# Kernel tuning notes

Measured on AMD Instinct MI355X. Metric: run time of the kernel, lower is better.

The kernel has to match this reference:

```python
import jax, jax.numpy as jnp
import numpy as np

BS, H, S, DK = 4, 16, 1024, 64  # bs, n_heads, seq_len(=q_len), head_dim


def setup_inputs() -> dict:
    key = jax.random.key(0)
    k1, k2, k3, k4 = jax.random.split(key, 4)
    return {
        "q": jax.random.normal(k1, (BS, H, S, DK), dtype=jnp.float32),
        "k": jax.random.normal(k2, (BS, H, DK, S), dtype=jnp.float32),
        "v": jax.random.normal(k3, (BS, H, S, DK), dtype=jnp.float32),
        "prev": jax.random.normal(k4, (BS, H, S, S), dtype=jnp.float32),
        "attn_mask": jnp.zeros((1, S, S), dtype=jnp.float32),  # additive float mask
        "key_padding_mask": jnp.zeros((BS, S), dtype=bool),     # True = masked key
        "scale": jnp.asarray(DK ** -0.5, dtype=jnp.float32),    # learnable (lsa=True)
    }


def reference(q, k, v, prev, attn_mask, key_padding_mask, scale):
    # attn_scores = q @ k * scale + prev + attn_mask (float branch)
    scores = jnp.einsum("bhqd,bhdk->bhqk", q, k) * scale
    scores = scores + prev + attn_mask[:, None, :, :]  # [1,S,S] -> broadcast over b,h
    # key_padding_mask: [bs, seq_len] -> masked_fill(-inf)
    scores = jnp.where(key_padding_mask[:, None, None, :], -jnp.inf, scores)
    attn = jax.nn.softmax(scores, axis=-1)  # dropout p=0.0 -> identity
    out = jnp.einsum("bhqk,bhkd->bhqd", attn, v)
    # res_attention=True -> (output, attn_weights, attn_scores)
    return out, attn, scores
```

## Files before the change

kernel.cpp:

```cpp
#include <hip/hip_runtime.h>
#include <math.h>

#define SEQ 1024
#define DKH 64
#define QBLK 64
#define NTILE 16
#define KSTR 68
#define ESTR 1032

typedef short s8v __attribute__((ext_vector_type(8)));
typedef short s4v __attribute__((ext_vector_type(4)));
typedef float f4v __attribute__((ext_vector_type(4)));

__device__ __forceinline__ short f2bf(float f) {
    unsigned u = __builtin_bit_cast(unsigned, f);
    return (short)((u + 0x8000u) >> 16);
}
__device__ __forceinline__ float bf2f(unsigned short h) {
    unsigned u = ((unsigned)h) << 16;
    return __builtin_bit_cast(float, u);
}
__device__ __forceinline__ s8v ld_frag(const unsigned short* p) {
    s4v a = *(const s4v*)(p);
    s4v b = *(const s4v*)(p + 4);
    s8v r;
    r[0]=a[0]; r[1]=a[1]; r[2]=a[2]; r[3]=a[3];
    r[4]=b[0]; r[5]=b[1]; r[6]=b[2]; r[7]=b[3];
    return r;
}

__global__ __launch_bounds__(256, 1)
void attn_fused(const float* __restrict__ q, const float* __restrict__ k,
                const float* __restrict__ v, const float* __restrict__ prev,
                const float* __restrict__ mask, const unsigned char* __restrict__ kpm,
                const float* __restrict__ scale_p,
                float* __restrict__ out, float* __restrict__ attn,
                float* __restrict__ scores)
{
    __shared__ unsigned short e_s[QBLK * ESTR];
    __shared__ unsigned short k_s[64 * KSTR];
    __shared__ unsigned short v_s[64 * KSTR];
    __shared__ float inv_s[QBLK];

    const int t   = threadIdx.x;
    const int w   = t >> 6;
    const int l   = t & 63;
    const int g   = l >> 4;
    const int c16 = l & 15;
    const int sa  = t & 15, sg = t >> 4;

    const int wg  = blockIdx.x;
    const int swz = (wg & 7) * 128 + (wg >> 3);
    const int bh  = swz >> 4;
    const int rt  = swz & 15;
    const int b   = bh >> 4;

    const float scale = *scale_p;

    const float* qb = q    + ((size_t)bh * SEQ + rt * QBLK) * DKH;
    const float* kb = k    + (size_t)bh * DKH * SEQ;
    const float* vb = v    + (size_t)bh * SEQ * DKH;
    const float* pb = prev + ((size_t)bh * SEQ + rt * QBLK) * SEQ;
    const float* mb = mask + (size_t)(rt * QBLK) * SEQ;
    const unsigned char* kp = kpm + (size_t)b * SEQ;
    float* sb = scores + ((size_t)bh * SEQ + rt * QBLK) * SEQ;
    float* ab = attn   + ((size_t)bh * SEQ + rt * QBLK) * SEQ;
    float* ob = out    + ((size_t)bh * SEQ + rt * QBLK) * DKH;

    {
        const int row = t >> 2, c0 = (t & 3) * 16;
        const float* src = qb + row * DKH + c0;
        #pragma unroll
        for (int j = 0; j < 4; ++j) {
            f4v f = *(const f4v*)(src + 4 * j);
            s4v h; h[0]=f2bf(f[0]); h[1]=f2bf(f[1]); h[2]=f2bf(f[2]); h[3]=f2bf(f[3]);
            *(s4v*)&e_s[row * ESTR + c0 + 4 * j] = h;
        }
    }
    __syncthreads();

    s8v aq[2];
    aq[0] = ld_frag(&e_s[(w * 16 + c16) * ESTR + g * 8]);
    aq[1] = ld_frag(&e_s[(w * 16 + c16) * ESTR + 32 + g * 8]);

    f4v kreg[4], vreg[4];
    auto load_k = [&](int ct) {
        const float* src = kb + (size_t)(4 * sg) * SEQ + ct * 64 + 4 * sa;
        kreg[0] = *(const f4v*)(src);
        kreg[1] = *(const f4v*)(src + SEQ);
        kreg[2] = *(const f4v*)(src + 2 * SEQ);
        kreg[3] = *(const f4v*)(src + 3 * SEQ);
    };
    auto load_v = [&](int ct) {
        const float* src = vb + (size_t)(ct * 64 + 4 * sg) * DKH + 4 * sa;
        vreg[0] = *(const f4v*)(src);
        vreg[1] = *(const f4v*)(src + DKH);
        vreg[2] = *(const f4v*)(src + 2 * DKH);
        vreg[3] = *(const f4v*)(src + 3 * DKH);
    };
    auto load_pm = [&](int ct, float (&pr)[16], float (&mr)[16]) {
        #pragma unroll
        for (int r = 0; r < 4; ++r) {
            const float* prow = pb + (size_t)(w * 16 + 4 * g + r) * SEQ + ct * 64 + c16;
            const float* mrow = mb + (size_t)(w * 16 + 4 * g + r) * SEQ + ct * 64 + c16;
            #pragma unroll
            for (int s = 0; s < 4; ++s) {
                pr[r * 4 + s] = __builtin_nontemporal_load(prow + s * 16);
                mr[r * 4 + s] = mrow[s * 16];
            }
        }
    };

    float l_r[4] = {0.f, 0.f, 0.f, 0.f};
    f4v oacc[4];
    #pragma unroll
    for (int d = 0; d < 4; ++d) oacc[d] = 0;

    float prA[16], mrA[16], prB[16], mrB[16];
    load_k(0); load_v(0);
    load_pm(0, prA, mrA);

    auto tile_body = [&](int ct, float (&prc)[16], float (&mrc)[16],
                         float (&prn)[16], float (&mrn)[16]) {
        __syncthreads();
        #pragma unroll
        for (int j = 0; j < 4; ++j) {
            s4v hk; hk[0]=f2bf(kreg[0][j]); hk[1]=f2bf(kreg[1][j]); hk[2]=f2bf(kreg[2][j]); hk[3]=f2bf(kreg[3][j]);
            *(s4v*)&k_s[(4 * sa + j) * KSTR + 4 * sg] = hk;
            s4v hv; hv[0]=f2bf(vreg[0][j]); hv[1]=f2bf(vreg[1][j]); hv[2]=f2bf(vreg[2][j]); hv[3]=f2bf(vreg[3][j]);
            *(s4v*)&v_s[(4 * sa + j) * KSTR + 4 * sg] = hv;
        }
        __syncthreads();

        if (ct + 1 < NTILE) {
            load_k(ct + 1); load_v(ct + 1);
            load_pm(ct + 1, prn, mrn);
        }

        f4v acc[4];
        #pragma unroll
        for (int s = 0; s < 4; ++s) acc[s] = 0;
        #pragma unroll
        for (int ks = 0; ks < 2; ++ks) {
            #pragma unroll
            for (int s = 0; s < 4; ++s) {
                s8v bk = ld_frag(&k_s[(s * 16 + c16) * KSTR + ks * 32 + g * 8]);
                acc[s] = __builtin_amdgcn_mfma_f32_16x16x32_bf16(aq[ks], bk, acc[s], 0, 0, 0);
            }
        }

        const int colb = ct * 64;
        int kf[4];
        #pragma unroll
        for (int s = 0; s < 4; ++s) kf[s] = kp[colb + s * 16 + c16];

        float ev[16];
        #pragma unroll
        for (int r = 0; r < 4; ++r) {
            float* srow = sb + (size_t)(w * 16 + 4 * g + r) * SEQ + colb + c16;
            #pragma unroll
            for (int s = 0; s < 4; ++s) {
                float x = fmaf(acc[s][r], scale, prc[r * 4 + s] + mrc[r * 4 + s]);
                x = kf[s] ? -INFINITY : x;
                __builtin_nontemporal_store(x, srow + s * 16);
                const float e = __expf(x);
                ev[r * 4 + s] = e;
                l_r[r] += e;
            }
        }
        #pragma unroll
        for (int r = 0; r < 4; ++r) {
            #pragma unroll
            for (int s = 0; s < 4; ++s)
                e_s[(w * 16 + 4 * g + r) * ESTR + colb + s * 16 + c16] =
                    (unsigned short)f2bf(ev[r * 4 + s]);
        }
        #pragma unroll
        for (int cs = 0; cs < 2; ++cs) {
            s8v ae = ld_frag(&e_s[(w * 16 + c16) * ESTR + colb + cs * 32 + g * 8]);
            #pragma unroll
            for (int d = 0; d < 4; ++d) {
                s8v bv = ld_frag(&v_s[(d * 16 + c16) * KSTR + cs * 32 + g * 8]);
                oacc[d] = __builtin_amdgcn_mfma_f32_16x16x32_bf16(ae, bv, oacc[d], 0, 0, 0);
            }
        }
    };

    for (int ct2 = 0; ct2 < NTILE; ct2 += 2) {
        tile_body(ct2,     prA, mrA, prB, mrB);
        tile_body(ct2 + 1, prB, mrB, prA, mrA);
    }

    #pragma unroll
    for (int off = 1; off <= 8; off <<= 1) {
        #pragma unroll
        for (int r = 0; r < 4; ++r) l_r[r] += __shfl_xor(l_r[r], off, 64);
    }
    float inv_r[4];
    #pragma unroll
    for (int r = 0; r < 4; ++r) inv_r[r] = 1.0f / l_r[r];
    if (c16 == 0) {
        #pragma unroll
        for (int r = 0; r < 4; ++r) inv_s[w * 16 + 4 * g + r] = inv_r[r];
    }

    const int rsub = l >> 4;
    #pragma unroll
    for (int rr = 0; rr < 4; ++rr) {
        const int row = w * 16 + rr * 4 + rsub;
        const float inv = inv_s[row];
        float* arow = ab + (size_t)row * SEQ;
        const unsigned short* erow = &e_s[row * ESTR];
        #pragma unroll
        for (int j = 0; j < 8; ++j) {
            const int c0 = j * 128 + c16 * 8;
            s8v h = ld_frag(erow + c0);
            f4v a0, a1;
            #pragma unroll
            for (int u = 0; u < 4; ++u) {
                a0[u] = bf2f((unsigned short)h[u]) * inv;
                a1[u] = bf2f((unsigned short)h[4 + u]) * inv;
            }
            __builtin_nontemporal_store(a0, (f4v*)(arow + c0));
            __builtin_nontemporal_store(a1, (f4v*)(arow + c0 + 4));
        }
    }

    #pragma unroll
    for (int d = 0; d < 4; ++d) {
        #pragma unroll
        for (int r = 0; r < 4; ++r)
            __builtin_nontemporal_store(oacc[d][r] * inv_r[r],
                ob + (size_t)(w * 16 + 4 * g + r) * DKH + d * 16 + c16);
    }
}

extern "C" void kernel_launch(void* const* d_in, const int* in_sizes, int n_in,
                              void* d_out, int out_size, void* d_ws, size_t ws_size,
                              hipStream_t stream) {
    const float* q    = (const float*)d_in[0];
    const float* k    = (const float*)d_in[1];
    const float* v    = (const float*)d_in[2];
    const float* prev = (const float*)d_in[3];
    const float* mask = (const float*)d_in[4];
    const unsigned char* kpm = (const unsigned char*)d_in[5];
    const float* scale = (const float*)d_in[6];

    float* out    = (float*)d_out;
    float* attn   = out  + (size_t)4 * 16 * SEQ * DKH;
    float* scores = attn + (size_t)4 * 16 * SEQ * SEQ;

    attn_fused<<<dim3(1024), dim3(256), 0, stream>>>(q, k, v, prev, mask, kpm, scale,
                                                     out, attn, scores);
}
```

Before: 294.5 us.

## Halve query block, use 8 waves splitting columns, load K/V fragments directly

```diff
diff --git a/kernel.cpp b/kernel.cpp
--- a/kernel.cpp
+++ b/kernel.cpp
@@ -3,10 +3,9 @@
 
 #define SEQ 1024
 #define DKH 64
-#define QBLK 64
+#define QBLK 32
 #define NTILE 16
-#define KSTR 68
-#define ESTR 1032
+#define ESTR 1028
 
 typedef short s8v __attribute__((ext_vector_type(8)));
 typedef short s4v __attribute__((ext_vector_type(4)));
@@ -29,7 +28,7 @@
     return r;
 }
 
-__global__ __launch_bounds__(256, 1)
+__global__ __launch_bounds__(512, 4)
 void attn_fused(const float* __restrict__ q, const float* __restrict__ k,
                 const float* __restrict__ v, const float* __restrict__ prev,
                 const float* __restrict__ mask, const unsigned char* __restrict__ kpm,
@@ -38,21 +37,21 @@
                 float* __restrict__ scores)
 {
     __shared__ unsigned short e_s[QBLK * ESTR];
-    __shared__ unsigned short k_s[64 * KSTR];
-    __shared__ unsigned short v_s[64 * KSTR];
+    __shared__ float l_part[QBLK][4];
     __shared__ float inv_s[QBLK];
 
     const int t   = threadIdx.x;
     const int w   = t >> 6;
+    const int rg  = w >> 2;
+    const int cq  = w & 3;
     const int l   = t & 63;
     const int g   = l >> 4;
     const int c16 = l & 15;
-    const int sa  = t & 15, sg = t >> 4;
 
     const int wg  = blockIdx.x;
-    const int swz = (wg & 7) * 128 + (wg >> 3);
-    const int bh  = swz >> 4;
-    const int rt  = swz & 15;
+    const int swz = (wg & 7) * 256 + (wg >> 3);
+    const int bh  = swz >> 5;
+    const int rt  = swz & 31;
     const int b   = bh >> 4;
 
     const float scale = *scale_p;
@@ -68,127 +67,92 @@
     float* ob = out    + ((size_t)bh * SEQ + rt * QBLK) * DKH;
 
     {
-        const int row = t >> 2, c0 = (t & 3) * 16;
-        const float* src = qb + row * DKH + c0;
-        #pragma unroll
-        for (int j = 0; j < 4; ++j) {
-            f4v f = *(const f4v*)(src + 4 * j);
-            s4v h; h[0]=f2bf(f[0]); h[1]=f2bf(f[1]); h[2]=f2bf(f[2]); h[3]=f2bf(f[3]);
-            *(s4v*)&e_s[row * ESTR + c0 + 4 * j] = h;
+        const int row = t >> 4, c0 = (t & 15) * 4;
+        f4v f = *(const f4v*)(qb + row * DKH + c0);
+        s4v h; h[0]=f2bf(f[0]); h[1]=f2bf(f[1]); h[2]=f2bf(f[2]); h[3]=f2bf(f[3]);
+        *(s4v*)&e_s[row * ESTR + c0] = h;
+    }
+    __syncthreads();
+
+    const s8v aq0 = ld_frag(&e_s[(rg * 16 + c16) * ESTR + g * 8]);
+    const s8v aq1 = ld_frag(&e_s[(rg * 16 + c16) * ESTR + 32 + g * 8]);
+    __syncthreads();
+
+    const float* kcol = kb + (size_t)(g * 8) * SEQ + cq * 16 + c16;
+    const float* vcol = vb + (size_t)(g * 8) * DKH + cq * 16 + c16;
+    const float* prow0 = pb + (size_t)(rg * 16 + g * 4) * SEQ + cq * 16 + c16;
+    const float* mrow0 = mb + (size_t)(rg * 16 + g * 4) * SEQ + cq * 16 + c16;
+
+    float kraw[16], vraw[16];
+    auto load_K = [&](int ct) {
+        const float* p0 = kcol + ct * 64;
+        #pragma unroll
+        for (int ks = 0; ks < 2; ++ks)
+            #pragma unroll
+            for (int e = 0; e < 8; ++e)
+                kraw[ks * 8 + e] = p0[(size_t)(ks * 32 + e) * SEQ];
+    };
+    auto load_V = [&](int ct) {
+        const float* p0 = vcol + (size_t)(ct * 64) * DKH;
+        #pragma unroll
+        for (int cs = 0; cs < 2; ++cs)
+            #pragma unroll
+            for (int e = 0; e < 8; ++e)
+                vraw[cs * 8 + e] = p0[(size_t)(cs * 32 + e) * DKH];
+    };
+    auto load_PM = [&](int ct, float (&pr)[4], float (&mr)[4], int& kf) {
+        #pragma unroll
+        for (int r = 0; r < 4; ++r) {
+            pr[r] = __builtin_nontemporal_load(prow0 + (size_t)r * SEQ + ct * 64);
+            mr[r] = mrow0[(size_t)r * SEQ + ct * 64];
         }
-    }
-    __syncthreads();
-
-    s8v aq[2];
-    aq[0] = ld_frag(&e_s[(w * 16 + c16) * ESTR + g * 8]);
-    aq[1] = ld_frag(&e_s[(w * 16 + c16) * ESTR + 32 + g * 8]);
-
-    f4v kreg[4], vreg[4];
-    auto load_k = [&](int ct) {
-        const float* src = kb + (size_t)(4 * sg) * SEQ + ct * 64 + 4 * sa;
-        kreg[0] = *(const f4v*)(src);
-        kreg[1] = *(const f4v*)(src + SEQ);
-        kreg[2] = *(const f4v*)(src + 2 * SEQ);
-        kreg[3] = *(const f4v*)(src + 3 * SEQ);
-    };
-    auto load_v = [&](int ct) {
-        const float* src = vb + (size_t)(ct * 64 + 4 * sg) * DKH + 4 * sa;
-        vreg[0] = *(const f4v*)(src);
-        vreg[1] = *(const f4v*)(src + DKH);
-        vreg[2] = *(const f4v*)(src + 2 * DKH);
-        vreg[3] = *(const f4v*)(src + 3 * DKH);
-    };
-    auto load_pm = [&](int ct, float (&pr)[16], float (&mr)[16]) {
+        kf = kp[ct * 64 + cq * 16 + c16];
+    };
+
+    float l_r[4] = {0.f, 0.f, 0.f, 0.f};
+    f4v oacc = 0;
+
+    float prA[4], mrA[4], prB[4], mrB[4];
+    int kfA = 0, kfB = 0;
+    load_K(0); load_V(0); load_PM(0, prA, mrA, kfA);
+
+    auto tile = [&](int ct, float (&prc)[4], float (&mrc)[4], int kfc,
+                    float (&prn)[4], float (&mrn)[4], int& kfn) {
+        s8v ka, kb2;
+        #pragma unroll
+        for (int e = 0; e < 8; ++e) { ka[e] = f2bf(kraw[e]); kb2[e] = f2bf(kraw[8 + e]); }
+        f4v acc = 0;
+        acc = __builtin_amdgcn_mfma_f32_16x16x32_bf16(aq0, ka,  acc, 0, 0, 0);
+        acc = __builtin_amdgcn_mfma_f32_16x16x32_bf16(aq1, kb2, acc, 0, 0, 0);
+        if (ct + 1 < NTILE) load_K(ct + 1);
+
+        const int colb = ct * 64 + cq * 16 + c16;
         #pragma unroll
         for (int r = 0; r < 4; ++r) {
-            const float* prow = pb + (size_t)(w * 16 + 4 * g + r) * SEQ + ct * 64 + c16;
-            const float* mrow = mb + (size_t)(w * 16 + 4 * g + r) * SEQ + ct * 64 + c16;
-            #pragma unroll
-            for (int s = 0; s < 4; ++s) {
-                pr[r * 4 + s] = __builtin_nontemporal_load(prow + s * 16);
-                mr[r * 4 + s] = mrow[s * 16];
-            }
+            const int row = rg * 16 + g * 4 + r;
+            float x = fmaf(acc[r], scale, prc[r] + mrc[r]);
+            x = kfc ? -INFINITY : x;
+            __builtin_nontemporal_store(x, sb + (size_t)row * SEQ + colb);
+            const float e = __expf(x);
+            l_r[r] += e;
+            e_s[row * ESTR + colb] = (unsigned short)f2bf(e);
         }
-    };
-
-    float l_r[4] = {0.f, 0.f, 0.f, 0.f};
-    f4v oacc[4];
-    #pragma unroll
-    for (int d = 0; d < 4; ++d) oacc[d] = 0;
-
-    float prA[16], mrA[16], prB[16], mrB[16];
-    load_k(0); load_v(0);
-    load_pm(0, prA, mrA);
-
-    auto tile_body = [&](int ct, float (&prc)[16], float (&mrc)[16],
-                         float (&prn)[16], float (&mrn)[16]) {
+        if (ct + 1 < NTILE) load_PM(ct + 1, prn, mrn, kfn);
         __syncthreads();
-        #pragma unroll
-        for (int j = 0; j < 4; ++j) {
-            s4v hk; hk[0]=f2bf(kreg[0][j]); hk[1]=f2bf(kreg[1][j]); hk[2]=f2bf(kreg[2][j]); hk[3]=f2bf(kreg[3][j]);
-            *(s4v*)&k_s[(4 * sa + j) * KSTR + 4 * sg] = hk;
-            s4v hv; hv[0]=f2bf(vreg[0][j]); hv[1]=f2bf(vreg[1][j]); hv[2]=f2bf(vreg[2][j]); hv[3]=f2bf(vreg[3][j]);
-            *(s4v*)&v_s[(4 * sa + j) * KSTR + 4 * sg] = hv;
-        }
-        __syncthreads();
-
-        if (ct + 1 < NTILE) {
-            load_k(ct + 1); load_v(ct + 1);
-            load_pm(ct + 1, prn, mrn);
-        }
-
-        f4v acc[4];
-        #pragma unroll
-        for (int s = 0; s < 4; ++s) acc[s] = 0;
-        #pragma unroll
-        for (int ks = 0; ks < 2; ++ks) {
-            #pragma unroll
-            for (int s = 0; s < 4; ++s) {
-                s8v bk = ld_frag(&k_s[(s * 16 + c16) * KSTR + ks * 32 + g * 8]);
-                acc[s] = __builtin_amdgcn_mfma_f32_16x16x32_bf16(aq[ks], bk, acc[s], 0, 0, 0);
-            }
-        }
-
-        const int colb = ct * 64;
-        int kf[4];
-        #pragma unroll
-        for (int s = 0; s < 4; ++s) kf[s] = kp[colb + s * 16 + c16];
-
-        float ev[16];
-        #pragma unroll
-        for (int r = 0; r < 4; ++r) {
-            float* srow = sb + (size_t)(w * 16 + 4 * g + r) * SEQ + colb + c16;
-            #pragma unroll
-            for (int s = 0; s < 4; ++s) {
-                float x = fmaf(acc[s][r], scale, prc[r * 4 + s] + mrc[r * 4 + s]);
-                x = kf[s] ? -INFINITY : x;
-                __builtin_nontemporal_store(x, srow + s * 16);
-                const float e = __expf(x);
-                ev[r * 4 + s] = e;
-                l_r[r] += e;
-            }
-        }
-        #pragma unroll
-        for (int r = 0; r < 4; ++r) {
-            #pragma unroll
-            for (int s = 0; s < 4; ++s)
-                e_s[(w * 16 + 4 * g + r) * ESTR + colb + s * 16 + c16] =
-                    (unsigned short)f2bf(ev[r * 4 + s]);
-        }
-        #pragma unroll
-        for (int cs = 0; cs < 2; ++cs) {
-            s8v ae = ld_frag(&e_s[(w * 16 + c16) * ESTR + colb + cs * 32 + g * 8]);
-            #pragma unroll
-            for (int d = 0; d < 4; ++d) {
-                s8v bv = ld_frag(&v_s[(d * 16 + c16) * KSTR + cs * 32 + g * 8]);
-                oacc[d] = __builtin_amdgcn_mfma_f32_16x16x32_bf16(ae, bv, oacc[d], 0, 0, 0);
-            }
-        }
-    };
-
-    for (int ct2 = 0; ct2 < NTILE; ct2 += 2) {
-        tile_body(ct2,     prA, mrA, prB, mrB);
-        tile_body(ct2 + 1, prB, mrB, prA, mrA);
+
+        const s8v ae0 = ld_frag(&e_s[(rg * 16 + c16) * ESTR + ct * 64 + g * 8]);
+        const s8v ae1 = ld_frag(&e_s[(rg * 16 + c16) * ESTR + ct * 64 + 32 + g * 8]);
+        s8v va, vb2;
+        #pragma unroll
+        for (int e = 0; e < 8; ++e) { va[e] = f2bf(vraw[e]); vb2[e] = f2bf(vraw[8 + e]); }
+        oacc = __builtin_amdgcn_mfma_f32_16x16x32_bf16(ae0, va,  oacc, 0, 0, 0);
+        oacc = __builtin_amdgcn_mfma_f32_16x16x32_bf16(ae1, vb2, oacc, 0, 0, 0);
+        if (ct + 1 < NTILE) load_V(ct + 1);
+    };
+
+    for (int c2 = 0; c2 < NTILE; c2 += 2) {
+        tile(c2,     prA, mrA, kfA, prB, mrB, kfB);
+        tile(c2 + 1, prB, mrB, kfB, prA, mrA, kfA);
     }
 
     #pragma unroll
@@ -196,24 +160,30 @@
         #pragma unroll
         for (int r = 0; r < 4; ++r) l_r[r] += __shfl_xor(l_r[r], off, 64);
     }
-    float inv_r[4];
+    if (c16 == 0) {
+        #pragma unroll
+        for (int r = 0; r < 4; ++r) l_part[rg * 16 + g * 4 + r][cq] = l_r[r];
+    }
+    __syncthreads();
+    if (t < QBLK)
+        inv_s[t] = 1.0f / (l_part[t][0] + l_part[t][1] + l_part[t][2] + l_part[t][3]);
+    __syncthreads();
+
     #pragma unroll
-    for (int r = 0; r < 4; ++r) inv_r[r] = 1.0f / l_r[r];
-    if (c16 == 0) {
-        #pragma unroll
-        for (int r = 0; r < 4; ++r) inv_s[w * 16 + 4 * g + r] = inv_r[r];
-    }
-
-    const int rsub = l >> 4;
-    #pragma unroll
-    for (int rr = 0; rr < 4; ++rr) {
-        const int row = w * 16 + rr * 4 + rsub;
+    for (int r = 0; r < 4; ++r) {
+        const int row = rg * 16 + g * 4 + r;
+        __builtin_nontemporal_store(oacc[r] * inv_s[row],
+            ob + (size_t)row * DKH + cq * 16 + c16);
+    }
+
+    {
+        const int row = t >> 4, i = t & 15;
         const float inv = inv_s[row];
+        const unsigned short* erow = &e_s[row * ESTR];
         float* arow = ab + (size_t)row * SEQ;
-        const unsigned short* erow = &e_s[row * ESTR];
         #pragma unroll
         for (int j = 0; j < 8; ++j) {
-            const int c0 = j * 128 + c16 * 8;
+            const int c0 = (j * 16 + i) * 8;
             s8v h = ld_frag(erow + c0);
             f4v a0, a1;
             #pragma unroll
@@ -225,14 +195,6 @@
             __builtin_nontemporal_store(a1, (f4v*)(arow + c0 + 4));
         }
     }
-
-    #pragma unroll
-    for (int d = 0; d < 4; ++d) {
-        #pragma unroll
-        for (int r = 0; r < 4; ++r)
-            __builtin_nontemporal_store(oacc[d][r] * inv_r[r],
-                ob + (size_t)(w * 16 + 4 * g + r) * DKH + d * 16 + c16);
-    }
 }
 
 extern "C" void kernel_launch(void* const* d_in, const int* in_sizes, int n_in,
@@ -250,6 +212,6 @@
     float* attn   = out  + (size_t)4 * 16 * SEQ * DKH;
     float* scores = attn + (size_t)4 * 16 * SEQ * SEQ;
 
-    attn_fused<<<dim3(1024), dim3(256), 0, stream>>>(q, k, v, prev, mask, kpm, scale,
+    attn_fused<<<dim3(2048), dim3(512), 0, stream>>>(q, k, v, prev, mask, kpm, scale,
                                                      out, attn, scores);
 }
```

New measurement: 326.5 us. 1.11x slower.

## Split fused attention into QK-scores kernel and PV/attn kernel for occupancy

Applied to the files above, without the earlier changes.

```diff
diff --git a/kernel.cpp b/kernel.cpp
--- a/kernel.cpp
+++ b/kernel.cpp
@@ -6,7 +6,6 @@
 #define QBLK 64
 #define NTILE 16
 #define KSTR 68
-#define ESTR 1032
 
 typedef short s8v __attribute__((ext_vector_type(8)));
 typedef short s4v __attribute__((ext_vector_type(4)));
@@ -15,10 +14,6 @@
 __device__ __forceinline__ short f2bf(float f) {
     unsigned u = __builtin_bit_cast(unsigned, f);
     return (short)((u + 0x8000u) >> 16);
-}
-__device__ __forceinline__ float bf2f(unsigned short h) {
-    unsigned u = ((unsigned)h) << 16;
-    return __builtin_bit_cast(float, u);
 }
 __device__ __forceinline__ s8v ld_frag(const unsigned short* p) {
     s4v a = *(const s4v*)(p);
@@ -29,18 +24,14 @@
     return r;
 }
 
-__global__ __launch_bounds__(256, 1)
-void attn_fused(const float* __restrict__ q, const float* __restrict__ k,
-                const float* __restrict__ v, const float* __restrict__ prev,
-                const float* __restrict__ mask, const unsigned char* __restrict__ kpm,
-                const float* __restrict__ scale_p,
-                float* __restrict__ out, float* __restrict__ attn,
-                float* __restrict__ scores)
+__global__ __launch_bounds__(256, 3)
+void qk_scores(const float* __restrict__ q, const float* __restrict__ k,
+               const float* __restrict__ prev, const float* __restrict__ mask,
+               const unsigned char* __restrict__ kpm, const float* __restrict__ scale_p,
+               float* __restrict__ scores, float* __restrict__ inv_ws)
 {
-    __shared__ unsigned short e_s[QBLK * ESTR];
+    __shared__ unsigned short q_s[QBLK * KSTR];
     __shared__ unsigned short k_s[64 * KSTR];
-    __shared__ unsigned short v_s[64 * KSTR];
-    __shared__ float inv_s[QBLK];
 
     const int t   = threadIdx.x;
     const int w   = t >> 6;
@@ -59,13 +50,10 @@
 
     const float* qb = q    + ((size_t)bh * SEQ + rt * QBLK) * DKH;
     const float* kb = k    + (size_t)bh * DKH * SEQ;
-    const float* vb = v    + (size_t)bh * SEQ * DKH;
     const float* pb = prev + ((size_t)bh * SEQ + rt * QBLK) * SEQ;
     const float* mb = mask + (size_t)(rt * QBLK) * SEQ;
     const unsigned char* kp = kpm + (size_t)b * SEQ;
     float* sb = scores + ((size_t)bh * SEQ + rt * QBLK) * SEQ;
-    float* ab = attn   + ((size_t)bh * SEQ + rt * QBLK) * SEQ;
-    float* ob = out    + ((size_t)bh * SEQ + rt * QBLK) * DKH;
 
     {
         const int row = t >> 2, c0 = (t & 3) * 16;
@@ -74,31 +62,22 @@
         for (int j = 0; j < 4; ++j) {
             f4v f = *(const f4v*)(src + 4 * j);
             s4v h; h[0]=f2bf(f[0]); h[1]=f2bf(f[1]); h[2]=f2bf(f[2]); h[3]=f2bf(f[3]);
-            *(s4v*)&e_s[row * ESTR + c0 + 4 * j] = h;
+            *(s4v*)&q_s[row * KSTR + c0 + 4 * j] = h;
         }
     }
     __syncthreads();
-
-    s8v aq[2];
-    aq[0] = ld_frag(&e_s[(w * 16 + c16) * ESTR + g * 8]);
-    aq[1] = ld_frag(&e_s[(w * 16 + c16) * ESTR + 32 + g * 8]);
-
-    f4v kreg[4], vreg[4];
-    auto load_k = [&](int ct) {
+    const s8v aq0 = ld_frag(&q_s[(w * 16 + c16) * KSTR + g * 8]);
+    const s8v aq1 = ld_frag(&q_s[(w * 16 + c16) * KSTR + 32 + g * 8]);
+
+    f4v kreg[4];
+    auto load_K = [&](int ct) {
         const float* src = kb + (size_t)(4 * sg) * SEQ + ct * 64 + 4 * sa;
         kreg[0] = *(const f4v*)(src);
         kreg[1] = *(const f4v*)(src + SEQ);
         kreg[2] = *(const f4v*)(src + 2 * SEQ);
         kreg[3] = *(const f4v*)(src + 3 * SEQ);
     };
-    auto load_v = [&](int ct) {
-        const float* src = vb + (size_t)(ct * 64 + 4 * sg) * DKH + 4 * sa;
-        vreg[0] = *(const f4v*)(src);
-        vreg[1] = *(const f4v*)(src + DKH);
-        vreg[2] = *(const f4v*)(src + 2 * DKH);
-        vreg[3] = *(const f4v*)(src + 3 * DKH);
-    };
-    auto load_pm = [&](int ct, float (&pr)[16], float (&mr)[16]) {
+    auto load_PM = [&](int ct, float (&pr)[16], float (&mr)[16], int (&kf)[4]) {
         #pragma unroll
         for (int r = 0; r < 4; ++r) {
             const float* prow = pb + (size_t)(w * 16 + 4 * g + r) * SEQ + ct * 64 + c16;
@@ -109,121 +88,163 @@
                 mr[r * 4 + s] = mrow[s * 16];
             }
         }
+        #pragma unroll
+        for (int s = 0; s < 4; ++s) kf[s] = kp[ct * 64 + s * 16 + c16];
     };
 
     float l_r[4] = {0.f, 0.f, 0.f, 0.f};
-    f4v oacc[4];
-    #pragma unroll
-    for (int d = 0; d < 4; ++d) oacc[d] = 0;
-
     float prA[16], mrA[16], prB[16], mrB[16];
-    load_k(0); load_v(0);
-    load_pm(0, prA, mrA);
-
-    auto tile_body = [&](int ct, float (&prc)[16], float (&mrc)[16],
-                         float (&prn)[16], float (&mrn)[16]) {
+    int kfA[4], kfB[4];
+    load_K(0);
+    load_PM(0, prA, mrA, kfA);
+
+    auto tile = [&](int ct, float (&prc)[16], float (&mrc)[16], int (&kfc)[4],
+                    float (&prn)[16], float (&mrn)[16], int (&kfn)[4]) {
         __syncthreads();
         #pragma unroll
         for (int j = 0; j < 4; ++j) {
             s4v hk; hk[0]=f2bf(kreg[0][j]); hk[1]=f2bf(kreg[1][j]); hk[2]=f2bf(kreg[2][j]); hk[3]=f2bf(kreg[3][j]);
             *(s4v*)&k_s[(4 * sa + j) * KSTR + 4 * sg] = hk;
-            s4v hv; hv[0]=f2bf(vreg[0][j]); hv[1]=f2bf(vreg[1][j]); hv[2]=f2bf(vreg[2][j]); hv[3]=f2bf(vreg[3][j]);
-            *(s4v*)&v_s[(4 * sa + j) * KSTR + 4 * sg] = hv;
-        }
-        __syncthreads();
-
-        if (ct + 1 < NTILE) {
-            load_k(ct + 1); load_v(ct + 1);
-            load_pm(ct + 1, prn, mrn);
-        }
+        }
+        __syncthreads();
+
+        if (ct + 1 < NTILE) load_K(ct + 1);
 
         f4v acc[4];
         #pragma unroll
         for (int s = 0; s < 4; ++s) acc[s] = 0;
         #pragma unroll
-        for (int ks = 0; ks < 2; ++ks) {
-            #pragma unroll
-            for (int s = 0; s < 4; ++s) {
-                s8v bk = ld_frag(&k_s[(s * 16 + c16) * KSTR + ks * 32 + g * 8]);
-                acc[s] = __builtin_amdgcn_mfma_f32_16x16x32_bf16(aq[ks], bk, acc[s], 0, 0, 0);
-            }
-        }
+        for (int s = 0; s < 4; ++s) {
+            const s8v bk0 = ld_frag(&k_s[(s * 16 + c16) * KSTR + g * 8]);
+            acc[s] = __builtin_amdgcn_mfma_f32_16x16x32_bf16(aq0, bk0, acc[s], 0, 0, 0);
+            const s8v bk1 = ld_frag(&k_s[(s * 16 + c16) * KSTR + 32 + g * 8]);
+            acc[s] = __builtin_amdgcn_mfma_f32_16x16x32_bf16(aq1, bk1, acc[s], 0, 0, 0);
+        }
+
+        if (ct + 1 < NTILE) load_PM(ct + 1, prn, mrn, kfn);
 
         const int colb = ct * 64;
-        int kf[4];
-        #pragma unroll
-        for (int s = 0; s < 4; ++s) kf[s] = kp[colb + s * 16 + c16];
-
-        float ev[16];
         #pragma unroll
         for (int r = 0; r < 4; ++r) {
             float* srow = sb + (size_t)(w * 16 + 4 * g + r) * SEQ + colb + c16;
             #pragma unroll
             for (int s = 0; s < 4; ++s) {
                 float x = fmaf(acc[s][r], scale, prc[r * 4 + s] + mrc[r * 4 + s]);
-                x = kf[s] ? -INFINITY : x;
-                __builtin_nontemporal_store(x, srow + s * 16);
-                const float e = __expf(x);
-                ev[r * 4 + s] = e;
-                l_r[r] += e;
+                x = kfc[s] ? -INFINITY : x;
+                srow[s * 16] = x;
+                l_r[r] += __expf(x);
             }
         }
+    };
+
+    for (int c2 = 0; c2 < NTILE; c2 += 2) {
+        tile(c2,     prA, mrA, kfA, prB, mrB, kfB);
+        tile(c2 + 1, prB, mrB, kfB, prA, mrA, kfA);
+    }
+
+    #pragma unroll
+    for (int off = 1; off <= 8; off <<= 1) {
+        #pragma unroll
+        for (int r = 0; r < 4; ++r) l_r[r] += __shfl_xor(l_r[r], off, 64);
+    }
+    if (c16 == 0) {
+        #pragma unroll
+        for (int r = 0; r < 4; ++r)
+            inv_ws[(size_t)bh * SEQ + rt * QBLK + w * 16 + 4 * g + r] = 1.0f / l_r[r];
+    }
+}
+
+__global__ __launch_bounds__(256, 3)
+void pv_attn(const float* __restrict__ v, const float* __restrict__ scores,
+             const float* __restrict__ inv_ws,
+             float* __restrict__ attn, float* __restrict__ out)
+{
+    __shared__ unsigned short v_s[64 * KSTR];
+    __shared__ unsigned short e_s[4][16 * KSTR];
+
+    const int t   = threadIdx.x;
+    const int w   = t >> 6;
+    const int l   = t & 63;
+    const int g   = l >> 4;
+    const int c16 = l & 15;
+    const int sa  = t & 15, sg = t >> 4;
+
+    const int wg  = blockIdx.x;
+    const int swz = (wg & 7) * 128 + (wg >> 3);
+    const int bh  = swz >> 4;
+    const int rt  = swz & 15;
+
+    const float* vb  = v      + (size_t)bh * SEQ * DKH;
+    const float* sbr = scores + ((size_t)bh * SEQ + rt * QBLK) * SEQ;
+    float* ab = attn + ((size_t)bh * SEQ + rt * QBLK) * SEQ;
+    float* ob = out  + ((size_t)bh * SEQ + rt * QBLK) * DKH;
+
+    float inv_r[4];
+    #pragma unroll
+    for (int r = 0; r < 4; ++r)
+        inv_r[r] = inv_ws[(size_t)bh * SEQ + rt * QBLK + w * 16 + g * 4 + r];
+
+    f4v vreg[4];
+    auto load_V = [&](int ct) {
+        const float* src = vb + (size_t)(ct * 64 + 4 * sg) * DKH + 4 * sa;
+        vreg[0] = *(const f4v*)(src);
+        vreg[1] = *(const f4v*)(src + DKH);
+        vreg[2] = *(const f4v*)(src + 2 * DKH);
+        vreg[3] = *(const f4v*)(src + 3 * DKH);
+    };
+    auto load_S = [&](int ct, f4v (&sr)[4]) {
+        #pragma unroll
+        for (int r = 0; r < 4; ++r)
+            sr[r] = *(const f4v*)(sbr + (size_t)(w * 16 + g * 4 + r) * SEQ + ct * 64 + c16 * 4);
+    };
+
+    f4v oacc[4];
+    #pragma unroll
+    for (int d = 0; d < 4; ++d) oacc[d] = 0;
+
+    f4v sregA[4], sregB[4];
+    load_V(0);
+    load_S(0, sregA);
+
+    auto tile = [&](int ct, f4v (&sc)[4], f4v (&sn)[4]) {
+        __syncthreads();
+        #pragma unroll
+        for (int j = 0; j < 4; ++j) {
+            s4v hv; hv[0]=f2bf(vreg[0][j]); hv[1]=f2bf(vreg[1][j]); hv[2]=f2bf(vreg[2][j]); hv[3]=f2bf(vreg[3][j]);
+            *(s4v*)&v_s[(4 * sa + j) * KSTR + 4 * sg] = hv;
+        }
+        __syncthreads();
+
+        if (ct + 1 < NTILE) { load_V(ct + 1); load_S(ct + 1, sn); }
+
         #pragma unroll
         for (int r = 0; r < 4; ++r) {
-            #pragma unroll
-            for (int s = 0; s < 4; ++s)
-                e_s[(w * 16 + 4 * g + r) * ESTR + colb + s * 16 + c16] =
-                    (unsigned short)f2bf(ev[r * 4 + s]);
-        }
-        #pragma unroll
-        for (int cs = 0; cs < 2; ++cs) {
-            s8v ae = ld_frag(&e_s[(w * 16 + c16) * ESTR + colb + cs * 32 + g * 8]);
+            const f4v s4 = sc[r];
+            const float e0 = __expf(s4[0]);
+            const float e1 = __expf(s4[1]);
+            const float e2 = __expf(s4[2]);
+            const float e3 = __expf(s4[3]);
+            f4v aw; aw[0]=e0*inv_r[r]; aw[1]=e1*inv_r[r]; aw[2]=e2*inv_r[r]; aw[3]=e3*inv_r[r];
+            __builtin_nontemporal_store(aw,
+                (f4v*)(ab + (size_t)(w * 16 + g * 4 + r) * SEQ + ct * 64 + c16 * 4));
+            s4v h; h[0]=f2bf(e0); h[1]=f2bf(e1); h[2]=f2bf(e2); h[3]=f2bf(e3);
+            *(s4v*)&e_s[w][(g * 4 + r) * KSTR + c16 * 4] = h;
+        }
+
+        #pragma unroll
+        for (int ks = 0; ks < 2; ++ks) {
+            const s8v ae = ld_frag(&e_s[w][c16 * KSTR + ks * 32 + g * 8]);
             #pragma unroll
             for (int d = 0; d < 4; ++d) {
-                s8v bv = ld_frag(&v_s[(d * 16 + c16) * KSTR + cs * 32 + g * 8]);
+                const s8v bv = ld_frag(&v_s[(d * 16 + c16) * KSTR + ks * 32 + g * 8]);
                 oacc[d] = __builtin_amdgcn_mfma_f32_16x16x32_bf16(ae, bv, oacc[d], 0, 0, 0);
             }
         }
     };
 
-    for (int ct2 = 0; ct2 < NTILE; ct2 += 2) {
-        tile_body(ct2,     prA, mrA, prB, mrB);
-        tile_body(ct2 + 1, prB, mrB, prA, mrA);
-    }
-
-    #pragma unroll
-    for (int off = 1; off <= 8; off <<= 1) {
-        #pragma unroll
-        for (int r = 0; r < 4; ++r) l_r[r] += __shfl_xor(l_r[r], off, 64);
-    }
-    float inv_r[4];
-    #pragma unroll
-    for (int r = 0; r < 4; ++r) inv_r[r] = 1.0f / l_r[r];
-    if (c16 == 0) {
-        #pragma unroll
-        for (int r = 0; r < 4; ++r) inv_s[w * 16 + 4 * g + r] = inv_r[r];
-    }
-
-    const int rsub = l >> 4;
-    #pragma unroll
-    for (int rr = 0; rr < 4; ++rr) {
-        const int row = w * 16 + rr * 4 + rsub;
-        const float inv = inv_s[row];
-        float* arow = ab + (size_t)row * SEQ;
-        const unsigned short* erow = &e_s[row * ESTR];
-        #pragma unroll
-        for (int j = 0; j < 8; ++j) {
-            const int c0 = j * 128 + c16 * 8;
-            s8v h = ld_frag(erow + c0);
-            f4v a0, a1;
-            #pragma unroll
-            for (int u = 0; u < 4; ++u) {
-                a0[u] = bf2f((unsigned short)h[u]) * inv;
-                a1[u] = bf2f((unsigned short)h[4 + u]) * inv;
-            }
-            __builtin_nontemporal_store(a0, (f4v*)(arow + c0));
-            __builtin_nontemporal_store(a1, (f4v*)(arow + c0 + 4));
-        }
+    for (int c2 = 0; c2 < NTILE; c2 += 2) {
+        tile(c2,     sregA, sregB);
+        tile(c2 + 1, sregB, sregA);
     }
 
     #pragma unroll
@@ -231,7 +252,7 @@
         #pragma unroll
         for (int r = 0; r < 4; ++r)
             __builtin_nontemporal_store(oacc[d][r] * inv_r[r],
-                ob + (size_t)(w * 16 + 4 * g + r) * DKH + d * 16 + c16);
+                ob + (size_t)(w * 16 + g * 4 + r) * DKH + d * 16 + c16);
     }
 }
 
@@ -249,7 +270,9 @@
     float* out    = (float*)d_out;
     float* attn   = out  + (size_t)4 * 16 * SEQ * DKH;
     float* scores = attn + (size_t)4 * 16 * SEQ * SEQ;
-
-    attn_fused<<<dim3(1024), dim3(256), 0, stream>>>(q, k, v, prev, mask, kpm, scale,
-                                                     out, attn, scores);
-}
+    float* inv_ws = (float*)d_ws;
+
+    qk_scores<<<dim3(1024), dim3(256), 0, stream>>>(q, k, prev, mask, kpm, scale,
+                                                    scores, inv_ws);
+    pv_attn<<<dim3(1024), dim3(256), 0, stream>>>(v, scores, inv_ws, attn, out);
+}
```

Result: faster. 276.9 us (-6.0%).
